# Optimization experiments

Measured on AMD Instinct MI355X. Metric: run time of the kernel, lower is better.

Reference implementation:

```python
import jax, jax.numpy as jnp
import numpy as np

N, F, T, H, E = 50000, 32, 16, 128, 800000
OUT = 1
EPS = 1e-5


def _lstm_layer(seq, Wih, Whh, bih, bhh):
    # seq: (T, N, Fin); PyTorch gate order i, f, g, o
    n = seq.shape[1]
    h0 = jnp.zeros((n, H), seq.dtype)
    c0 = jnp.zeros((n, H), seq.dtype)

    def step(carry, xt):
        h, c = carry
        z = xt @ Wih.T + h @ Whh.T + (bih + bhh)
        i, f, g, o = jnp.split(z, 4, axis=-1)
        c = jax.nn.sigmoid(f) * c + jax.nn.sigmoid(i) * jnp.tanh(g)
        h = jax.nn.sigmoid(o) * jnp.tanh(c)
        return (h, c), h

    (h_last, _), hs = jax.lax.scan(step, (h0, c0), seq)
    return hs, h_last


def _layernorm(x, gamma, beta):
    mu = jnp.mean(x, axis=-1, keepdims=True)
    var = jnp.mean(jnp.square(x - mu), axis=-1, keepdims=True)
    return (x - mu) * jax.lax.rsqrt(var + EPS) * gamma + beta


def _gcn(x, W, b, src, dst, w, n):
    # PyG GCNConv with self-loops already appended to (src, dst, w)
    deg = jax.ops.segment_sum(w, dst, num_segments=n)
    dinv = jnp.where(deg > 0, jax.lax.rsqrt(deg), 0.0)
    norm = dinv[src] * w * dinv[dst]  # (E+N,)
    h = x @ W  # (n, H)
    msg = h[src] * norm[:, None]
    return jax.ops.segment_sum(msg, dst, num_segments=n) + b


def setup_inputs() -> dict:
    key = jax.random.key(0)
    ks = jax.random.split(key, 24)
    s = 0.05
    inp = {
        "x": jax.random.normal(ks[0], (N, F, T), jnp.float32),
        "edge_index": jax.random.randint(ks[1], (2, E), 0, N, jnp.int32),
        "edge_weight": jax.random.uniform(ks[2], (E,), jnp.float32),
        # LSTM layer 0
        "Wih0": jax.random.normal(ks[3], (4 * H, F), jnp.float32) * s,
        "Whh0": jax.random.normal(ks[4], (4 * H, H), jnp.float32) * s,
        "bih0": jnp.zeros((4 * H,), jnp.float32),
        "bhh0": jnp.zeros((4 * H,), jnp.float32),
        # LSTM layer 1
        "Wih1": jax.random.normal(ks[5], (4 * H, H), jnp.float32) * s,
        "Whh1": jax.random.normal(ks[6], (4 * H, H), jnp.float32) * s,
        "bih1": jnp.zeros((4 * H,), jnp.float32),
        "bhh1": jnp.zeros((4 * H,), jnp.float32),
        # GCN layers + LayerNorms
        "Wg1": jax.random.normal(ks[7], (H, H), jnp.float32) * s,
        "bg1": jnp.zeros((H,), jnp.float32),
        "g1": jnp.ones((H,), jnp.float32),
        "be1": jnp.zeros((H,), jnp.float32),
        "Wg2": jax.random.normal(ks[8], (H, H), jnp.float32) * s,
        "bg2": jnp.zeros((H,), jnp.float32),
        "g2": jnp.ones((H,), jnp.float32),
        "be2": jnp.zeros((H,), jnp.float32),
        # Predictor: Linear(2H, H//2) -> ReLU -> Linear(H//2, 1)
        "Wp1": jax.random.normal(ks[9], (2 * H, H // 2), jnp.float32) * s,
        "bp1": jnp.zeros((H // 2,), jnp.float32),
        "Wp2": jax.random.normal(ks[10], (H // 2, OUT), jnp.float32) * s,
        "bp2": jnp.zeros((OUT,), jnp.float32),
    }
    return inp


def reference(x, edge_index, edge_weight, Wih0, Whh0, bih0, bhh0,
              Wih1, Whh1, bih1, bhh1, Wg1, bg1, g1, be1,
              Wg2, bg2, g2, be2, Wp1, bp1, Wp2, bp2):
    n = x.shape[0]
    # Temporal encoder: (N, F, T) -> transpose(1,2) -> seq over T
    seq = jnp.transpose(x, (2, 0, 1))  # (T, N, F)
    hs0, _ = _lstm_layer(seq, Wih0, Whh0, bih0, bhh0)  # (T, N, H)
    _, temporal = _lstm_layer(hs0, Wih1, Whh1, bih1, bhh1)  # (N, H)

    # Graph encoder (GCN x2 with self-loops + LayerNorm; ReLU between)
    loops = jnp.arange(n, dtype=edge_index.dtype)
    src = jnp.concatenate([edge_index[0], loops])
    dst = jnp.concatenate([edge_index[1], loops])
    w = jnp.concatenate([edge_weight, jnp.ones((n,), edge_weight.dtype)])
    h = _gcn(temporal, Wg1, bg1, src, dst, w, n)
    h = jax.nn.relu(_layernorm(h, g1, be1))  # dropout: eval no-op
    h = _gcn(h, Wg2, bg2, src, dst, w, n)
    graph_feat = _layernorm(h, g2, be2)

    # Fusion (concat) + predictor
    fused = jnp.concatenate([temporal, graph_feat], axis=1)  # (N, 2H)
    hid = jax.nn.relu(fused @ Wp1 + bp1)
    return hid @ Wp2 + bp2
```

## Files before the change

### kernel.cpp

```cpp
#include <hip/hip_runtime.h>
#include <math.h>

#define Hdim 128
#define Fdim 32
#define Tdim 16

typedef short  bfrag8 __attribute__((ext_vector_type(8)));
typedef float  facc4  __attribute__((ext_vector_type(4)));
typedef unsigned short ushort_t;

__device__ __forceinline__ float sigf(float x) {
    return 1.0f / (1.0f + __expf(-x));
}
__device__ __forceinline__ float tanh_fast(float x) {
    x = fminf(fmaxf(x, -15.f), 15.f);
    float e = __expf(2.f * x);
    return (e - 1.f) / (e + 1.f);
}
__device__ __forceinline__ ushort_t f2bf(float f) {
    union { float f; unsigned u; } v; v.f = f;
    unsigned u = v.u;
    unsigned r = u + 0x7fffu + ((u >> 16) & 1u);
    return (ushort_t)(r >> 16);
}

__global__ __launch_bounds__(256)
void cvt_bf16_kernel(const float* __restrict__ in, ushort_t* __restrict__ out, int nelem) {
    int i = (blockIdx.x * 256 + threadIdx.x) * 4;
    if (i < nelem) {
        float4 v = *reinterpret_cast<const float4*>(in + i);
        out[i + 0] = f2bf(v.x); out[i + 1] = f2bf(v.y);
        out[i + 2] = f2bf(v.z); out[i + 3] = f2bf(v.w);
    }
}

__global__ __launch_bounds__(256)
void bias_add_kernel(const float* __restrict__ a, const float* __restrict__ b,
                     float* __restrict__ out, int n) {
    int i = blockIdx.x * 256 + threadIdx.x;
    if (i < n) out[i] = a[i] + b[i];
}

__global__ __launch_bounds__(256)
void transpose_x_kernel(const float* __restrict__ x, ushort_t* __restrict__ xs, int nf) {
    int tid = blockIdx.x * 256 + threadIdx.x;
    if (tid >= nf) return;
    const float4* src = reinterpret_cast<const float4*>(x + (size_t)tid * Tdim);
    float4 a = src[0], b = src[1], c = src[2], d = src[3];
    float v[16] = {a.x,a.y,a.z,a.w, b.x,b.y,b.z,b.w, c.x,c.y,c.z,c.w, d.x,d.y,d.z,d.w};
    #pragma unroll
    for (int t = 0; t < Tdim; ++t) xs[(size_t)t * nf + tid] = f2bf(v[t]);
}

__global__ __launch_bounds__(256)
void xslice_kernel(const float* __restrict__ x, ushort_t* __restrict__ xt, int t, int n) {
    int idx = blockIdx.x * 256 + threadIdx.x;
    if (idx < n * Fdim) {
        int node = idx >> 5, f = idx & 31;
        xt[idx] = f2bf(x[(size_t)node * (Fdim * Tdim) + f * Tdim + t]);
    }
}

template<int Kp>
__device__ __forceinline__ void lstm_phase_lds(
    const ushort_t* __restrict__ Ap, const ushort_t* __restrict__ Wp,
    ushort_t* __restrict__ As, ushort_t* __restrict__ Bs,
    facc4 (&acc)[4][4],
    int rb_blk, int jb_blk, int wr, int wc, int rl, int ks, int tid, int n)
{
    #pragma unroll
    for (int k0 = 0; k0 < Kp; k0 += 32) {
        __syncthreads();
        #pragma unroll
        for (int s = 0; s < 2; ++s) {
            const int slot = tid + 256 * s;
            const int arow = slot >> 2;
            const int c8   = (slot & 3) * 8;
            int grow = rb_blk + arow; grow = grow < n ? grow : n - 1;
            bfrag8 av = *reinterpret_cast<const bfrag8*>(
                Ap + (size_t)grow * Kp + k0 + c8);
            const int g = arow >> 5, j = arow & 31;
            bfrag8 bv = *reinterpret_cast<const bfrag8*>(
                Wp + (size_t)(g * Hdim + jb_blk + j) * Kp + k0 + c8);
            *reinterpret_cast<bfrag8*>(As + slot * 8) = av;
            *reinterpret_cast<bfrag8*>(Bs + slot * 8) = bv;
        }
        __syncthreads();
        bfrag8 bfr[4];
        #pragma unroll
        for (int g = 0; g < 4; ++g)
            bfr[g] = *reinterpret_cast<const bfrag8*>(
                Bs + ((g * 32 + wc * 16 + rl) * 32 + ks * 8));
        #pragma unroll
        for (int m = 0; m < 4; ++m) {
            bfrag8 afr = *reinterpret_cast<const bfrag8*>(
                As + ((wr * 64 + m * 16 + rl) * 32 + ks * 8));
            #pragma unroll
            for (int g = 0; g < 4; ++g)
                acc[m][g] = __builtin_amdgcn_mfma_f32_16x16x32_bf16(
                    afr, bfr[g], acc[m][g], 0, 0, 0);
        }
    }
}

template<int KX>
__device__ __forceinline__
void lstm_step_core(const ushort_t* __restrict__ xt, const ushort_t* __restrict__ h_in,
                    float* __restrict__ c_state,
                    const ushort_t* __restrict__ Wx, const ushort_t* __restrict__ Wh,
                    const float* __restrict__ bias,
                    ushort_t* __restrict__ h_out, float* __restrict__ h_f32,
                    ushort_t* __restrict__ As, ushort_t* __restrict__ Bs,
                    int n, int bx, int by)
{
    const int tid  = threadIdx.x;
    const int lane = tid & 63;
    const int w    = tid >> 6;
    const int wr   = w >> 1, wc = w & 1;
    const int rb_blk = bx * 128;
    const int jb_blk = by * 32;
    const int rl   = lane & 15;
    const int ks   = lane >> 4;

    facc4 acc[4][4] = {};

    lstm_phase_lds<KX>(xt, Wx, As, Bs, acc, rb_blk, jb_blk, wr, wc, rl, ks, tid, n);
    lstm_phase_lds<Hdim>(h_in, Wh, As, Bs, acc, rb_blk, jb_blk, wr, wc, rl, ks, tid, n);

    const int rb = rb_blk + wr * 64;
    const int jj = jb_blk + wc * 16 + rl;
    const float bi = bias[jj];
    const float bf_ = bias[Hdim + jj];
    const float bg = bias[2 * Hdim + jj];
    const float bo = bias[3 * Hdim + jj];
    #pragma unroll
    for (int m = 0; m < 4; ++m) {
        #pragma unroll
        for (int j = 0; j < 4; ++j) {
            const int r = rb + m * 16 + ks * 4 + j;
            if (r < n) {
                const size_t idx = (size_t)r * Hdim + jj;
                const float zi = acc[m][0][j] + bi;
                const float zf = acc[m][1][j] + bf_;
                const float zg = acc[m][2][j] + bg;
                const float zo = acc[m][3][j] + bo;
                const float co = c_state[idx];
                const float cn = sigf(zf) * co + sigf(zi) * tanh_fast(zg);
                c_state[idx] = cn;
                const float h = sigf(zo) * tanh_fast(cn);
                h_out[idx] = f2bf(h);
                if (h_f32 != nullptr) h_f32[idx] = h;
            }
        }
    }
}

__global__ __launch_bounds__(256)
void lstm_pair_kernel(const ushort_t* __restrict__ xt,
                      const ushort_t* __restrict__ h0_in, ushort_t* __restrict__ h0_out,
                      float* __restrict__ c0,
                      const ushort_t* __restrict__ Wx0, const ushort_t* __restrict__ Wh0,
                      const float* __restrict__ b0,
                      const ushort_t* __restrict__ h1_in, ushort_t* __restrict__ h1_out,
                      float* __restrict__ c1,
                      const ushort_t* __restrict__ Wx1, const ushort_t* __restrict__ Wh1,
                      const float* __restrict__ b1,
                      float* __restrict__ temporal_or_null, int t, int n)
{
    __shared__ ushort_t As[128 * 32];
    __shared__ ushort_t Bs[128 * 32];
    if (blockIdx.z == 0) {
        if (t >= Tdim) return;
        lstm_step_core<Fdim>(xt, h0_in, c0, Wx0, Wh0, b0, h0_out, nullptr,
                             As, Bs, n, blockIdx.x, blockIdx.y);
    } else {
        if (t == 0) return;
        lstm_step_core<Hdim>(h0_in, h1_in, c1, Wx1, Wh1, b1, h1_out, temporal_or_null,
                             As, Bs, n, blockIdx.x, blockIdx.y);
    }
}

__global__ __launch_bounds__(256)
void gemm_h_kernel(const float* __restrict__ A, const float* __restrict__ B,
                   float* __restrict__ C, int n)
{
    __shared__ float As[32][68];
    __shared__ float Bs[32][128];
    const int tid = threadIdx.x;
    const int jx = tid & 31;
    const int ry = tid >> 5;
    const int rowbase = blockIdx.x * 64;
    float acc[8][4];
    #pragma unroll
    for (int r = 0; r < 8; ++r)
        #pragma unroll
        for (int q = 0; q < 4; ++q) acc[r][q] = 0.f;

    for (int k0 = 0; k0 < 128; k0 += 32) {
        {
            const int kq = tid & 7, row = tid >> 3;
            #pragma unroll
            for (int hh = 0; hh < 2; ++hh) {
                const int r = row + hh * 32;
                const int grow = rowbase + r;
                float4 v = make_float4(0.f, 0.f, 0.f, 0.f);
                if (grow < n) v = *reinterpret_cast<const float4*>(
                                    A + (size_t)grow * 128 + k0 + kq * 4);
                As[kq*4+0][r] = v.x; As[kq*4+1][r] = v.y;
                As[kq*4+2][r] = v.z; As[kq*4+3][r] = v.w;
            }
        }
        {
            const float4* src = reinterpret_cast<const float4*>(B + (size_t)k0 * 128);
            float4* dst = reinterpret_cast<float4*>(&Bs[0][0]);
            for (int i = tid; i < 1024; i += 256) dst[i] = src[i];
        }
        __syncthreads();
        #pragma unroll
        for (int k = 0; k < 32; ++k) {
            float a[8];
            float4 a0 = *reinterpret_cast<const float4*>(&As[k][ry * 8]);
            float4 a1 = *reinterpret_cast<const float4*>(&As[k][ry * 8 + 4]);
            a[0]=a0.x; a[1]=a0.y; a[2]=a0.z; a[3]=a0.w;
            a[4]=a1.x; a[5]=a1.y; a[6]=a1.z; a[7]=a1.w;
            const float b0 = Bs[k][jx], b1 = Bs[k][jx+32];
            const float b2 = Bs[k][jx+64], b3 = Bs[k][jx+96];
            #pragma unroll
            for (int r = 0; r < 8; ++r) {
                acc[r][0] = fmaf(a[r], b0, acc[r][0]);
                acc[r][1] = fmaf(a[r], b1, acc[r][1]);
                acc[r][2] = fmaf(a[r], b2, acc[r][2]);
                acc[r][3] = fmaf(a[r], b3, acc[r][3]);
            }
        }
        __syncthreads();
    }
    #pragma unroll
    for (int r = 0; r < 8; ++r) {
        const int grow = rowbase + ry * 8 + r;
        if (grow < n) {
            #pragma unroll
            for (int q = 0; q < 4; ++q)
                C[(size_t)grow * 128 + jx + q * 32] = acc[r][q];
        }
    }
}

__global__ __launch_bounds__(256)
void deg_hist_kernel(const int* __restrict__ dst, const float* __restrict__ w,
                     float* deg, int* counts, int E) {
    int e = blockIdx.x * 256 + threadIdx.x;
    if (e < E) {
        int d = dst[e];
        atomicAdd(&deg[d], w[e]);
        atomicAdd(&counts[d], 1);
    }
}

__global__ __launch_bounds__(256)
void dinv_kernel(float* deg_dinv, int n) {
    int i = blockIdx.x * 256 + threadIdx.x;
    if (i < n) deg_dinv[i] = rsqrtf(deg_dinv[i] + 1.0f);
}

__global__ __launch_bounds__(256)
void scan1_kernel(const int* __restrict__ counts, int* __restrict__ Sloc,
                  int* __restrict__ bsum, int n) {
    __shared__ int tmp[256];
    const int i = blockIdx.x * 256 + threadIdx.x;
    tmp[threadIdx.x] = (i < n) ? counts[i] : 0;
    __syncthreads();
    #pragma unroll
    for (int off = 1; off < 256; off <<= 1) {
        int t = (threadIdx.x >= off) ? tmp[threadIdx.x - off] : 0;
        __syncthreads();
        tmp[threadIdx.x] += t;
        __syncthreads();
    }
    if (i < n) Sloc[i] = tmp[threadIdx.x];
    if (threadIdx.x == 255) bsum[blockIdx.x] = tmp[255];
}

__global__ __launch_bounds__(256)
void scan2_kernel(int* __restrict__ bsum, int nb) {
    __shared__ int tmp[256];
    tmp[threadIdx.x] = (threadIdx.x < nb) ? bsum[threadIdx.x] : 0;
    __syncthreads();
    #pragma unroll
    for (int off = 1; off < 256; off <<= 1) {
        int t = (threadIdx.x >= off) ? tmp[threadIdx.x - off] : 0;
        __syncthreads();
        tmp[threadIdx.x] += t;
        __syncthreads();
    }
    if (threadIdx.x < nb) bsum[threadIdx.x] = tmp[threadIdx.x];
}

__global__ __launch_bounds__(256)
void scan3_kernel(const int* __restrict__ Sloc, const int* __restrict__ bsum,
                  const int* __restrict__ counts,
                  int* __restrict__ rowstart, int* __restrict__ running, int n) {
    const int i = blockIdx.x * 256 + threadIdx.x;
    if (i >= n) return;
    const int S = Sloc[i] + (blockIdx.x > 0 ? bsum[blockIdx.x - 1] : 0);
    const int rs = S - counts[i];
    rowstart[i] = rs;
    running[i]  = rs;
}

__global__ __launch_bounds__(256)
void scatter_kernel(const int* __restrict__ src, const int* __restrict__ dst,
                    const float* __restrict__ w, const float* __restrict__ dinv,
                    int* __restrict__ running,
                    int* __restrict__ s_srt, float* __restrict__ w_srt, int E) {
    int e = blockIdx.x * 256 + threadIdx.x;
    if (e >= E) return;
    const int s = src[e], d = dst[e];
    const int pos = atomicAdd(&running[d], 1);
    s_srt[pos] = s;
    w_srt[pos] = dinv[s] * w[e] * dinv[d];
}

template<bool RELU>
__global__ __launch_bounds__(256)
void gather_ln_kernel(const float* __restrict__ hlin,
                      const int* __restrict__ rowstart, const int* __restrict__ counts,
                      const int* __restrict__ s_srt, const float* __restrict__ w_srt,
                      const float* __restrict__ dinv, const float* __restrict__ bias,
                      const float* __restrict__ gamma, const float* __restrict__ beta,
                      float* __restrict__ out, int n)
{
    const int wave = threadIdx.x >> 6;
    const int lane = threadIdx.x & 63;
    const int node = blockIdx.x * 4 + wave;
    if (node >= n) return;

    const float di = dinv[node];
    float a0 = hlin[(size_t)node * Hdim + lane]      * di * di + bias[lane];
    float a1 = hlin[(size_t)node * Hdim + 64 + lane] * di * di + bias[64 + lane];

    const int rs  = rowstart[node];
    const int cnt = counts[node];
    int j = rs;
    const int jend = rs + cnt;
    for (; j + 1 < jend; j += 2) {
        const int   sA = s_srt[j],     sB = s_srt[j + 1];
        const float wA = w_srt[j],     wB = w_srt[j + 1];
        const float* rA = hlin + (size_t)sA * Hdim;
        const float* rB = hlin + (size_t)sB * Hdim;
        a0 += rA[lane] * wA;      a1 += rA[64 + lane] * wA;
        a0 += rB[lane] * wB;      a1 += rB[64 + lane] * wB;
    }
    if (j < jend) {
        const int   sA = s_srt[j];
        const float wA = w_srt[j];
        const float* rA = hlin + (size_t)sA * Hdim;
        a0 += rA[lane] * wA;      a1 += rA[64 + lane] * wA;
    }

    float s = a0 + a1;
    #pragma unroll
    for (int m = 32; m >= 1; m >>= 1) s += __shfl_xor(s, m);
    const float mu = s * (1.f / 128.f);
    const float d0 = a0 - mu, d1 = a1 - mu;
    float v = d0 * d0 + d1 * d1;
    #pragma unroll
    for (int m = 32; m >= 1; m >>= 1) v += __shfl_xor(v, m);
    const float rstd = rsqrtf(v * (1.f / 128.f) + 1e-5f);
    float y0 = d0 * rstd * gamma[lane]      + beta[lane];
    float y1 = d1 * rstd * gamma[64 + lane] + beta[64 + lane];
    if (RELU) { y0 = fmaxf(y0, 0.f); y1 = fmaxf(y1, 0.f); }
    out[(size_t)node * Hdim + lane]      = y0;
    out[(size_t)node * Hdim + 64 + lane] = y1;
}

__global__ __launch_bounds__(256)
void predictor_kernel(const float* __restrict__ temporal, const float* __restrict__ gfeat,
                      const float* __restrict__ Wp1, const float* __restrict__ bp1,
                      const float* __restrict__ Wp2, const float* __restrict__ bp2,
                      float* __restrict__ out, int n)
{
    const int node = blockIdx.x * 256 + threadIdx.x;
    const int nd = node < n ? node : n - 1;
    float acc[64];
    #pragma unroll
    for (int l = 0; l < 64; ++l) acc[l] = bp1[l];
    #pragma unroll
    for (int half = 0; half < 2; ++half) {
        const float* src = (half == 0 ? temporal : gfeat) + (size_t)nd * 128;
        const float* Wh_ = Wp1 + half * 128 * 64;
        for (int k4 = 0; k4 < 32; ++k4) {
            const float4 f = reinterpret_cast<const float4*>(src)[k4];
            const float fe[4] = { f.x, f.y, f.z, f.w };
            #pragma unroll
            for (int e = 0; e < 4; ++e) {
                const float* wr = Wh_ + (k4 * 4 + e) * 64;
                #pragma unroll
                for (int l = 0; l < 64; ++l)
                    acc[l] = fmaf(fe[e], wr[l], acc[l]);
            }
        }
    }
    float p = bp2[0];
    #pragma unroll
    for (int l = 0; l < 64; ++l)
        p = fmaf(fmaxf(acc[l], 0.f), Wp2[l], p);
    if (node < n) out[node] = p;
}

extern "C" void kernel_launch(void* const* d_in, const int* in_sizes, int n_in,
                              void* d_out, int out_size, void* d_ws, size_t ws_size,
                              hipStream_t stream) {
    const float* x    = (const float*)d_in[0];
    const int*   ei   = (const int*)d_in[1];
    const float* ew   = (const float*)d_in[2];
    const float* Wih0 = (const float*)d_in[3];
    const float* Whh0 = (const float*)d_in[4];
    const float* bih0 = (const float*)d_in[5];
    const float* bhh0 = (const float*)d_in[6];
    const float* Wih1 = (const float*)d_in[7];
    const float* Whh1 = (const float*)d_in[8];
    const float* bih1 = (const float*)d_in[9];
    const float* bhh1 = (const float*)d_in[10];
    const float* Wg1  = (const float*)d_in[11];
    const float* bg1  = (const float*)d_in[12];
    const float* g1   = (const float*)d_in[13];
    const float* be1  = (const float*)d_in[14];
    const float* Wg2  = (const float*)d_in[15];
    const float* bg2  = (const float*)d_in[16];
    const float* g2   = (const float*)d_in[17];
    const float* be2  = (const float*)d_in[18];
    const float* Wp1  = (const float*)d_in[19];
    const float* bp1  = (const float*)d_in[20];
    const float* Wp2  = (const float*)d_in[21];
    const float* bp2  = (const float*)d_in[22];
    float* out = (float*)d_out;

    const int n = in_sizes[0] / (Fdim * Tdim);
    const int E = in_sizes[1] / 2;
    const int* esrc = ei;
    const int* edst = ei + E;

    const size_t NH = (size_t)n * Hdim;
    const size_t NF = (size_t)n * Fdim;

    const size_t wsz_weights = (size_t)(512 * Fdim + 3 * 512 * Hdim) * 2;
    const size_t csr_bytes = (size_t)n * 16 + (size_t)E * 8 + 2048;
    const size_t need_rest = 4 * (NH * 2)
                           + 2 * (NH * 4)
                           + (NH * 4)
                           + (size_t)n * 4
                           + wsz_weights + 2 * 512 * 4 + csr_bytes + 16384;
    const bool use_xs = ws_size >= NF * Tdim * 2 + need_rest;

    char* base = (char*)d_ws;
    size_t off = 0;
    auto alloc = [&](size_t bytes) -> char* {
        off = (off + 255) & ~(size_t)255;
        char* p = base + off;
        off += bytes;
        return p;
    };
    ushort_t* xs   = (ushort_t*)alloc(use_xs ? NF * Tdim * 2 : NF * 2);
    ushort_t* h0a  = (ushort_t*)alloc(NH * 2);
    ushort_t* h0b  = (ushort_t*)alloc(NH * 2);
    ushort_t* h1a  = (ushort_t*)alloc(NH * 2);
    ushort_t* h1b  = (ushort_t*)alloc(NH * 2);
    float*    c0   = (float*)alloc(NH * 4);
    float*    c1   = (float*)alloc(NH * 4);
    float*    temporal = (float*)alloc(NH * 4);
    float*    dinv = (float*)alloc((size_t)n * 4);
    ushort_t* Wx0b = (ushort_t*)alloc((size_t)512 * Fdim * 2);
    ushort_t* Wh0b = (ushort_t*)alloc((size_t)512 * Hdim * 2);
    ushort_t* Wx1b = (ushort_t*)alloc((size_t)512 * Hdim * 2);
    ushort_t* Wh1b = (ushort_t*)alloc((size_t)512 * Hdim * 2);
    float*    bias0 = (float*)alloc(512 * 4);
    float*    bias1 = (float*)alloc(512 * 4);
    int*   counts   = (int*)alloc((size_t)n * 4);
    int*   Sloc     = (int*)alloc((size_t)n * 4);
    int*   bsum     = (int*)alloc(1024);
    int*   rowstart = (int*)alloc((size_t)n * 4);
    int*   running  = (int*)alloc((size_t)n * 4);
    int*   s_srt    = (int*)alloc((size_t)E * 4);
    float* w_srt    = (float*)alloc((size_t)E * 4);
    float* G1 = (float*)base;
    float* G2 = G1 + NH;
    float* G3 = G2 + NH;

    {
        const int n0 = 512 * Fdim, n1 = 512 * Hdim;
        cvt_bf16_kernel<<<(n0/4 + 255)/256, 256, 0, stream>>>(Wih0, Wx0b, n0);
        cvt_bf16_kernel<<<(n1/4 + 255)/256, 256, 0, stream>>>(Whh0, Wh0b, n1);
        cvt_bf16_kernel<<<(n1/4 + 255)/256, 256, 0, stream>>>(Wih1, Wx1b, n1);
        cvt_bf16_kernel<<<(n1/4 + 255)/256, 256, 0, stream>>>(Whh1, Wh1b, n1);
        bias_add_kernel<<<2, 256, 0, stream>>>(bih0, bhh0, bias0, 512);
        bias_add_kernel<<<2, 256, 0, stream>>>(bih1, bhh1, bias1, 512);
    }

    hipMemsetAsync(h0a, 0, NH * 2, stream);
    hipMemsetAsync(h1a, 0, NH * 2, stream);
    hipMemsetAsync(c0, 0, NH * 4, stream);
    hipMemsetAsync(c1, 0, NH * 4, stream);
    hipMemsetAsync(dinv, 0, (size_t)n * 4, stream);
    hipMemsetAsync(counts, 0, (size_t)n * 4, stream);

    {
        const int eb = (E + 255) / 256;
        const int nb = (n + 255) / 256;
        deg_hist_kernel<<<eb, 256, 0, stream>>>(edst, ew, dinv, counts, E);
        dinv_kernel<<<nb, 256, 0, stream>>>(dinv, n);
        scan1_kernel<<<nb, 256, 0, stream>>>(counts, Sloc, bsum, n);
        scan2_kernel<<<1, 256, 0, stream>>>(bsum, nb);
        scan3_kernel<<<nb, 256, 0, stream>>>(Sloc, bsum, counts, rowstart, running, n);
        scatter_kernel<<<eb, 256, 0, stream>>>(esrc, edst, ew, dinv, running,
                                               s_srt, w_srt, E);
    }

    if (use_xs)
        transpose_x_kernel<<<(int)((NF + 255) / 256), 256, 0, stream>>>(x, xs, (int)NF);

    ushort_t* B[2] = { h0a, h0b };
    ushort_t* H[2] = { h1a, h1b };
    dim3 lgrid((n + 127) / 128, 4, 2);
    for (int t = 0; t <= Tdim; ++t) {
        const ushort_t* xt = xs;
        if (t < Tdim) {
            if (use_xs) xt = xs + (size_t)t * NF;
            else {
                xslice_kernel<<<(int)((NF + 255) / 256), 256, 0, stream>>>(x, xs, t, n);
                xt = xs;
            }
        }
        float* tf32 = (t == Tdim) ? temporal : nullptr;
        lstm_pair_kernel<<<lgrid, 256, 0, stream>>>(
            xt, B[t & 1], B[(t + 1) & 1], c0, Wx0b, Wh0b, bias0,
            H[(t + 1) & 1], H[t & 1], c1, Wx1b, Wh1b, bias1,
            tf32, t, n);
    }

    const int gblocks  = (n + 63) / 64;
    const int nwblocks = (n + 3) / 4;
    gemm_h_kernel<<<gblocks, 256, 0, stream>>>(temporal, Wg1, G1, n);
    gather_ln_kernel<true><<<nwblocks, 256, 0, stream>>>(
        G1, rowstart, counts, s_srt, w_srt, dinv, bg1, g1, be1, G3, n);
    gemm_h_kernel<<<gblocks, 256, 0, stream>>>(G3, Wg2, G1, n);
    gather_ln_kernel<false><<<nwblocks, 256, 0, stream>>>(
        G1, rowstart, counts, s_srt, w_srt, dinv, bg2, g2, be2, G2, n);

    predictor_kernel<<<(n + 255) / 256, 256, 0, stream>>>(
        temporal, G2, Wp1, bp1, Wp2, bp2, out, n);
}
```

Measured before the change: 1.791 ms.

## Double-buffer LSTM GEMM tiles via direct global-to-LDS loads; stage predictor weights in LDS

The LSTM step kernel now fuses the input and recurrent K loops into a single iteration space. Each tile is copied straight into one of two LDS buffers with global_load_lds, so the next tile's load overlaps the current MFMA work and one of the two barriers per iteration goes away. Separately, the predictor kernel copies Wp1 (64 KB) into shared memory and reads it with float4 vector loads instead of scalar global loads. The cost is doubled LDS for the LSTM kernel and 64 KB of LDS per predictor block, which may lower occupancy.

```diff
diff --git a/kernel.cpp b/kernel.cpp
--- a/kernel.cpp
+++ b/kernel.cpp
@@ -22,6 +22,12 @@
     unsigned u = v.u;
     unsigned r = u + 0x7fffu + ((u >> 16) & 1u);
     return (ushort_t)(r >> 16);
+}
+
+typedef __attribute__((address_space(3))) unsigned int lds_uint;
+typedef __attribute__((address_space(1))) const unsigned int glob_uint;
+__device__ __forceinline__ void gload_lds16(const ushort_t* g, ushort_t* l) {
+    __builtin_amdgcn_global_load_lds((glob_uint*)g, (lds_uint*)l, 16, 0, 0);
 }
 
 __global__ __launch_bounds__(256)
@@ -61,46 +67,15 @@
     }
 }
 
-template<int Kp>
-__device__ __forceinline__ void lstm_phase_lds(
-    const ushort_t* __restrict__ Ap, const ushort_t* __restrict__ Wp,
-    ushort_t* __restrict__ As, ushort_t* __restrict__ Bs,
-    facc4 (&acc)[4][4],
-    int rb_blk, int jb_blk, int wr, int wc, int rl, int ks, int tid, int n)
+template<int KX>
+__device__ __forceinline__
+void get_iter(int gi, const ushort_t* xt, const ushort_t* h_in,
+              const ushort_t* Wx, const ushort_t* Wh,
+              const ushort_t*& Ap, const ushort_t*& Wp, int& Kp, int& k0)
 {
-    #pragma unroll
-    for (int k0 = 0; k0 < Kp; k0 += 32) {
-        __syncthreads();
-        #pragma unroll
-        for (int s = 0; s < 2; ++s) {
-            const int slot = tid + 256 * s;
-            const int arow = slot >> 2;
-            const int c8   = (slot & 3) * 8;
-            int grow = rb_blk + arow; grow = grow < n ? grow : n - 1;
-            bfrag8 av = *reinterpret_cast<const bfrag8*>(
-                Ap + (size_t)grow * Kp + k0 + c8);
-            const int g = arow >> 5, j = arow & 31;
-            bfrag8 bv = *reinterpret_cast<const bfrag8*>(
-                Wp + (size_t)(g * Hdim + jb_blk + j) * Kp + k0 + c8);
-            *reinterpret_cast<bfrag8*>(As + slot * 8) = av;
-            *reinterpret_cast<bfrag8*>(Bs + slot * 8) = bv;
-        }
-        __syncthreads();
-        bfrag8 bfr[4];
-        #pragma unroll
-        for (int g = 0; g < 4; ++g)
-            bfr[g] = *reinterpret_cast<const bfrag8*>(
-                Bs + ((g * 32 + wc * 16 + rl) * 32 + ks * 8));
-        #pragma unroll
-        for (int m = 0; m < 4; ++m) {
-            bfrag8 afr = *reinterpret_cast<const bfrag8*>(
-                As + ((wr * 64 + m * 16 + rl) * 32 + ks * 8));
-            #pragma unroll
-            for (int g = 0; g < 4; ++g)
-                acc[m][g] = __builtin_amdgcn_mfma_f32_16x16x32_bf16(
-                    afr, bfr[g], acc[m][g], 0, 0, 0);
-        }
-    }
+    constexpr int itX = KX / 32;
+    if (gi < itX) { Ap = xt;   Wp = Wx; Kp = KX;   k0 = gi * 32; }
+    else          { Ap = h_in; Wp = Wh; Kp = Hdim; k0 = (gi - itX) * 32; }
 }
 
 template<int KX>
@@ -110,9 +85,10 @@
                     const ushort_t* __restrict__ Wx, const ushort_t* __restrict__ Wh,
                     const float* __restrict__ bias,
                     ushort_t* __restrict__ h_out, float* __restrict__ h_f32,
-                    ushort_t* __restrict__ As, ushort_t* __restrict__ Bs,
+                    ushort_t (*As)[4096], ushort_t (*Bs)[4096],
                     int n, int bx, int by)
 {
+    constexpr int NIT = KX / 32 + 4;
     const int tid  = threadIdx.x;
     const int lane = tid & 63;
     const int w    = tid >> 6;
@@ -121,11 +97,48 @@
     const int jb_blk = by * 32;
     const int rl   = lane & 15;
     const int ks   = lane >> 4;
+    const int sub  = lane >> 2;
+    const int boff = (lane & 3) * 8;
+
+    auto stage = [&](int gi, int b) {
+        const ushort_t *Ap, *Wp; int Kp, k0;
+        get_iter<KX>(gi, xt, h_in, Wx, Wh, Ap, Wp, Kp, k0);
+        #pragma unroll
+        for (int h = 0; h < 2; ++h) {
+            const int r = w * 32 + h * 16 + sub;
+            int growA = rb_blk + r; growA = growA < n ? growA : n - 1;
+            gload_lds16(Ap + (size_t)growA * Kp + k0 + boff,
+                        As[b] + (w * 32 + h * 16) * 32);
+            const int g = r >> 5, j = r & 31;
+            gload_lds16(Wp + (size_t)(g * Hdim + jb_blk + j) * Kp + k0 + boff,
+                        Bs[b] + (w * 32 + h * 16) * 32);
+        }
+    };
 
     facc4 acc[4][4] = {};
 
-    lstm_phase_lds<KX>(xt, Wx, As, Bs, acc, rb_blk, jb_blk, wr, wc, rl, ks, tid, n);
-    lstm_phase_lds<Hdim>(h_in, Wh, As, Bs, acc, rb_blk, jb_blk, wr, wc, rl, ks, tid, n);
+    stage(0, 0);
+    __syncthreads();
+    #pragma unroll
+    for (int gi = 0; gi < NIT; ++gi) {
+        const int cur = gi & 1;
+        if (gi + 1 < NIT) stage(gi + 1, cur ^ 1);
+        bfrag8 bfr[4];
+        #pragma unroll
+        for (int g = 0; g < 4; ++g)
+            bfr[g] = *reinterpret_cast<const bfrag8*>(
+                Bs[cur] + ((g * 32 + wc * 16 + rl) * 32 + ks * 8));
+        #pragma unroll
+        for (int m = 0; m < 4; ++m) {
+            bfrag8 afr = *reinterpret_cast<const bfrag8*>(
+                As[cur] + ((wr * 64 + m * 16 + rl) * 32 + ks * 8));
+            #pragma unroll
+            for (int g = 0; g < 4; ++g)
+                acc[m][g] = __builtin_amdgcn_mfma_f32_16x16x32_bf16(
+                    afr, bfr[g], acc[m][g], 0, 0, 0);
+        }
+        __syncthreads();
+    }
 
     const int rb = rb_blk + wr * 64;
     const int jj = jb_blk + wc * 16 + rl;
@@ -167,8 +180,8 @@
                       const float* __restrict__ b1,
                       float* __restrict__ temporal_or_null, int t, int n)
 {
-    __shared__ ushort_t As[128 * 32];
-    __shared__ ushort_t Bs[128 * 32];
+    __shared__ ushort_t As[2][4096];
+    __shared__ ushort_t Bs[2][4096];
     if (blockIdx.z == 0) {
         if (t >= Tdim) return;
         lstm_step_core<Fdim>(xt, h0_in, c0, Wx0, Wh0, b0, h0_out, nullptr,
@@ -380,24 +393,38 @@
                       const float* __restrict__ Wp2, const float* __restrict__ bp2,
                       float* __restrict__ out, int n)
 {
-    const int node = blockIdx.x * 256 + threadIdx.x;
+    __shared__ float Ws[256 * 64];
+    const int tid = threadIdx.x;
+    {
+        const float4* src = reinterpret_cast<const float4*>(Wp1);
+        float4* dst = reinterpret_cast<float4*>(Ws);
+        for (int i = tid; i < 4096; i += 256) dst[i] = src[i];
+    }
+    __syncthreads();
+    const int node = blockIdx.x * 256 + tid;
     const int nd = node < n ? node : n - 1;
     float acc[64];
     #pragma unroll
     for (int l = 0; l < 64; ++l) acc[l] = bp1[l];
     #pragma unroll
     for (int half = 0; half < 2; ++half) {
-        const float* src = (half == 0 ? temporal : gfeat) + (size_t)nd * 128;
-        const float* Wh_ = Wp1 + half * 128 * 64;
+        const float* srcp = (half == 0 ? temporal : gfeat) + (size_t)nd * 128;
+        #pragma unroll 4
         for (int k4 = 0; k4 < 32; ++k4) {
-            const float4 f = reinterpret_cast<const float4*>(src)[k4];
+            const float4 f = reinterpret_cast<const float4*>(srcp)[k4];
             const float fe[4] = { f.x, f.y, f.z, f.w };
             #pragma unroll
             for (int e = 0; e < 4; ++e) {
-                const float* wr = Wh_ + (k4 * 4 + e) * 64;
+                const float4* wrow = reinterpret_cast<const float4*>(
+                    Ws + (half * 128 + k4 * 4 + e) * 64);
                 #pragma unroll
-                for (int l = 0; l < 64; ++l)
-                    acc[l] = fmaf(fe[e], wr[l], acc[l]);
+                for (int l4 = 0; l4 < 16; ++l4) {
+                    const float4 wv = wrow[l4];
+                    acc[l4*4+0] = fmaf(fe[e], wv.x, acc[l4*4+0]);
+                    acc[l4*4+1] = fmaf(fe[e], wv.y, acc[l4*4+1]);
+                    acc[l4*4+2] = fmaf(fe[e], wv.z, acc[l4*4+2]);
+                    acc[l4*4+3] = fmaf(fe[e], wv.w, acc[l4*4+3]);
+                }
             }
         }
     }
```

Result: no change. 1.761 ms (-1.6%).
